# Kernel optimization log

Hardware: AMD Instinct MI355X
Metric: run time of the kernel (lower is better)

Reference implementation:

```python
import jax, jax.numpy as jnp
import numpy as np

N, E, G = 8192, 65536, 16          # nodes, edges, graphs
EMBED, HID, L = 512, 1024, 3       # embed_dim, hidden_dim, hidden_layers
NG, RBF_R = 50, 12.0               # num_gaussians, rbf_radius
AVG_LEN = 60.0
IN_DIM = 3 * EMBED


def _mlp_params(key, in_dim, hid, out_dim, n_layers):
    ks = jax.random.split(key, 6)
    s_in = 1.0 / np.sqrt(in_dim)
    s_h = 1.0 / np.sqrt(hid)
    return dict(
        in_w=jax.random.normal(ks[0], (in_dim, hid), jnp.float32) * s_in,
        in_b=jnp.zeros((hid,), jnp.float32),
        hid_w=jax.random.normal(ks[1], (n_layers, hid, hid), jnp.float32) * s_h,
        hid_b=jnp.zeros((n_layers, hid), jnp.float32),
        out_w=jax.random.normal(ks[2], (hid, out_dim), jnp.float32) * s_h,
        out_b=jnp.zeros((out_dim,), jnp.float32),
    )


def setup_inputs() -> dict:
    key = jax.random.key(0)
    k = jax.random.split(key, 8)
    x = jax.random.normal(k[0], (N, EMBED), jnp.float32)
    edge_index = jax.random.randint(k[1], (2, E), 0, N, dtype=jnp.int32)
    batch = jnp.sort(jax.random.randint(k[2], (N,), 0, G, dtype=jnp.int32))
    dist = jax.random.uniform(k[3], (E,), jnp.float32) * RBF_R
    v = jax.random.normal(k[4], (E, 3), jnp.float32)
    vec_hat = v / jnp.linalg.norm(v, axis=-1, keepdims=True)
    rbf_w = jax.random.normal(k[5], (NG, EMBED), jnp.float32) * (1.0 / np.sqrt(NG))
    rbf_b = jnp.zeros((EMBED,), jnp.float32)
    e = _mlp_params(k[6], IN_DIM, HID, 1, L)
    f = _mlp_params(k[7], IN_DIM, HID, 1, L)
    return dict(
        x=x, edge_index=edge_index, batch=batch, dist=dist, vec_hat=vec_hat,
        rbf_w=rbf_w, rbf_b=rbf_b,
        e_in_w=e['in_w'], e_in_b=e['in_b'], e_hid_w=e['hid_w'], e_hid_b=e['hid_b'], e_out_w=e['out_w'], e_out_b=e['out_b'],
        f_in_w=f['in_w'], f_in_b=f['in_b'], f_hid_w=f['hid_w'], f_hid_b=f['hid_b'], f_out_w=f['out_w'], f_out_b=f['out_b'],
    )


def _res_mlp(h_in, in_w, in_b, hid_w, hid_b, out_w, out_b):
    h = jax.nn.silu(h_in @ in_w + in_b)           # [E, HID]
    for i in range(L):                             # residual hidden blocks
        h = h + jax.nn.silu(h @ hid_w[i] + hid_b[i])
    return h @ out_w + out_b                       # [E, 1]


def _rbf(dist, rbf_w, rbf_b):
    offsets = jnp.linspace(0.0, RBF_R, NG)
    coeff = -0.5 / (offsets[1] - offsets[0]) ** 2
    g = jnp.exp(coeff * (dist[:, None] - offsets) ** 2)  # [E, NG]
    return g @ rbf_w + rbf_b                              # [E, EMBED]


def reference(x, edge_index, batch, dist, vec_hat,
              rbf_w, rbf_b,
              e_in_w, e_in_b, e_hid_w, e_hid_b, e_out_w, e_out_b,
              f_in_w, f_in_b, f_hid_w, f_hid_b, f_out_w, f_out_b):
    src, dst = edge_index[0], edge_index[1]
    rbf = _rbf(dist, rbf_w, rbf_b)                                 # [E, EMBED]
    inputs = jnp.concatenate([x[src], x[dst], rbf], axis=-1)       # [E, 3*EMBED]
    energy_pairs = _res_mlp(inputs, e_in_w, e_in_b, e_hid_w, e_hid_b, e_out_w, e_out_b)  # [E,1]
    force_pairs = _res_mlp(inputs, f_in_w, f_in_b, f_hid_w, f_hid_b, f_out_w, f_out_b) * vec_hat  # [E,3]
    energy = jax.ops.segment_sum(energy_pairs, batch[src], num_segments=G) / (AVG_LEN ** 2)  # [G,1]
    forces = jax.ops.segment_sum(force_pairs, src, num_segments=N) / AVG_LEN                 # [N,3]
    return energy, forces
```

## Files before the change

### kernel.cpp

```cpp
#include <hip/hip_runtime.h>
#include <math.h>

#define NUM_E 65536
#define NUM_N 8192
#define NUM_G 16
#define RBFR 12.0f

typedef unsigned short u16;
typedef _Float16 f16x8 __attribute__((ext_vector_type(8)));
typedef _Float16 f16x4 __attribute__((ext_vector_type(4)));
typedef float f32x4 __attribute__((ext_vector_type(4)));

#define TILE_F16 8192
#define L1SZ   1114112
#define HSZ    1048576
#define MSTRIDE 4259840

#define FU1  139264
#define FUHL 131072
#define FUPM (FU1 + 3 * FUHL)

#define GLD16(gp, lp) __builtin_amdgcn_global_load_lds( \
    (const __attribute__((address_space(1))) void*)(gp), \
    (__attribute__((address_space(3))) void*)(lp), 16, 0, 0)

#define VMW12() asm volatile("s_waitcnt vmcnt(12)" ::: "memory")
#define VMW10() asm volatile("s_waitcnt vmcnt(10)" ::: "memory")
#define VMW8()  asm volatile("s_waitcnt vmcnt(8)" ::: "memory")
#define VMW0()  asm volatile("s_waitcnt vmcnt(0)" ::: "memory")
#define BARX()  __builtin_amdgcn_s_barrier()

__global__ void wrbf_kernel(const float* __restrict__ rbf_w, const float* __restrict__ rbf_b,
                            const float* __restrict__ e_in_w, const float* __restrict__ e_in_b,
                            const float* __restrict__ f_in_w, const float* __restrict__ f_in_b,
                            float* __restrict__ wrbf_e, float* __restrict__ b1_e,
                            float* __restrict__ wrbf_f, float* __restrict__ b1_f) {
  int blk = blockIdx.x;
  int mlp = blk / 51;
  int row = blk % 51;
  const float* in_w = mlp ? f_in_w : e_in_w;
  const float* in_b = mlp ? f_in_b : e_in_b;
  float* wrbf = mlp ? wrbf_f : wrbf_e;
  float* b1   = mlp ? b1_f : b1_e;
  __shared__ float vec[512];
  for (int i = threadIdx.x; i < 512; i += 256)
    vec[i] = (row < 50) ? rbf_w[row * 512 + i] : rbf_b[i];
  __syncthreads();
  int n0 = threadIdx.x * 4;
  float a0 = 0.f, a1 = 0.f, a2 = 0.f, a3 = 0.f;
  for (int c = 0; c < 512; ++c) {
    const float4 wv = *(const float4*)&in_w[(size_t)(1024 + c) * 1024 + n0];
    float g = vec[c];
    a0 += g * wv.x; a1 += g * wv.y; a2 += g * wv.z; a3 += g * wv.w;
  }
  if (row < 50) {
    float4 o = {a0, a1, a2, a3};
    *(float4*)&wrbf[row * 1024 + n0] = o;
  } else {
    float4 o = {a0 + in_b[n0], a1 + in_b[n0 + 1], a2 + in_b[n0 + 2], a3 + in_b[n0 + 3]};
    *(float4*)&b1[n0] = o;
  }
}

__global__ void xh_kernel(const float* __restrict__ x, u16* __restrict__ xh) {
  int i = blockIdx.x * 256 + threadIdx.x;
  float4 v = ((const float4*)x)[i];
  f16x4 h = {(_Float16)v.x, (_Float16)v.y, (_Float16)v.z, (_Float16)v.w};
  *(f16x4*)(xh + (size_t)i * 4) = h;
}

__global__ void grbf_kernel(const float* __restrict__ dist, u16* __restrict__ grbf) {
  int u = blockIdx.x * 256 + threadIdx.x;
  int e = u >> 3, q = u & 7;
  const float delta = RBFR / 49.f;
  const float coeff = -0.5f / (delta * delta);
  float d = dist[e];
  f16x8 h;
#pragma unroll
  for (int j = 0; j < 8; ++j) {
    int gi = q * 8 + j;
    float dd = d - (float)gi * delta;
    float gg = (gi < 50) ? __expf(coeff * dd * dd) : 0.f;
    h[j] = (_Float16)gg;
  }
  *(f16x8*)(grbf + (size_t)u * 8) = h;
}

__global__ void pack_gemm(const float* __restrict__ e_in_w, const float* __restrict__ e_hid_w,
                          const float* __restrict__ f_in_w, const float* __restrict__ f_hid_w,
                          const float* __restrict__ wrbf_e, const float* __restrict__ wrbf_f,
                          u16* __restrict__ wp) {
  int u = blockIdx.x * 256 + threadIdx.x;
  if (u >= 2 * (MSTRIDE / 8)) return;
  int mlpi = (u >= MSTRIDE / 8) ? 1 : 0;
  int v = u - mlpi * (MSTRIDE / 8);
  const float* in_w  = mlpi ? f_in_w : e_in_w;
  const float* hid_w = mlpi ? f_hid_w : e_hid_w;
  const float* wrbf  = mlpi ? wrbf_f : wrbf_e;
  int t = v >> 10;
  int unit = v & 1023;
  int n_loc = unit >> 3;
  int sp = unit & 7;
  int ks = sp ^ (n_loc & 7);
  f16x8 vals;
  if (t < 136) {
    int grp = t / 17;
    int kt = t % 17;
    int bnp = grp >> 1, nhp = grp & 1;
    int n = bnp * 256 + ((n_loc >> 5) << 6) + nhp * 32 + (n_loc & 31);
    int k0 = kt * 64 + ks * 8;
#pragma unroll
    for (int j = 0; j < 8; ++j) {
      int k = k0 + j;
      float f = (k < 1024) ? in_w[(size_t)k * 1024 + n]
              : ((k < 1074) ? wrbf[(k - 1024) * 1024 + n] : 0.f);
      vals[j] = (_Float16)f;
    }
  } else {
    int th = t - 136;
    int lay = th >> 7;
    int t2 = th & 127;
    int bnp = t2 >> 5;
    int nhp = (t2 >> 4) & 1;
    int kt = t2 & 15;
    int n = bnp * 256 + ((n_loc >> 5) << 6) + nhp * 32 + (n_loc & 31);
    int k0 = kt * 64 + ks * 8;
#pragma unroll
    for (int j = 0; j < 8; ++j)
      vals[j] = (_Float16)hid_w[(size_t)((lay << 10) + k0 + j) * 1024 + n];
  }
  *(f16x8*)(wp + (size_t)mlpi * MSTRIDE + (size_t)t * TILE_F16 + unit * 8) = vals;
}


#define STA(b, ah, kt) do { \
  _Pragma("unroll") for (int _j = 0; _j < 2; ++_j) { \
    int _ck = wv * 2 + _j; \
    int _loc = _ck * 8 + (lane >> 3); \
    int _row = ((_loc >> 6) << 7) + (ah) * 64 + (_loc & 63); \
    int _sw = ((lane & 7) ^ (_loc & 7)) << 3; \
    const u16* _gp; \
    if (ISL1) { \
      if ((kt) < 16) { \
        int _nd = ((kt) < 8) ? s_src[_row] : s_dst[_row]; \
        _gp = hin + ((size_t)_nd * 512 + ((kt) & 7) * 64 + _sw); \
      } else { \
        _gp = grbf + ((size_t)(eg0 + _row) * 64 + _sw); \
      } \
    } else { \
      _gp = hin + ((size_t)(rowb + _row) * 1024 + (kt) * 64 + _sw); \
    } \
    GLD16(_gp, (char*)&sm[b][ah][0] + _ck * 1024); \
  } \
} while (0)

#define STB(b, bh, kt) do { \
  const u16* _wt = wl + ((size_t)((bn * 2 + (bh)) * NKT + (kt))) * TILE_F16; \
  _Pragma("unroll") for (int _j = 0; _j < 2; ++_j) { \
    int _ck = wv * 2 + _j; \
    GLD16(_wt + _ck * 512 + lane * 8, (char*)&sm[b][2 + (bh)][0] + _ck * 1024); \
  } \
} while (0)

#define RDA(b, mh) do { \
  _Pragma("unroll") for (int _ks = 0; _ks < 2; ++_ks) { \
    int _kk = _ks * 4 + (lane >> 4); \
    _Pragma("unroll") for (int _m = 0; _m < 4; ++_m) { \
      int _r = wm * 64 + _m * 16 + (lane & 15); \
      af[_m][_ks] = *(const f16x8*)&sm[b][mh][_r * 64 + ((_kk ^ (_r & 7)) << 3)]; \
    } \
  } \
} while (0)

#define RDB(b, nh) do { \
  _Pragma("unroll") for (int _ks = 0; _ks < 2; ++_ks) { \
    int _kk = _ks * 4 + (lane >> 4); \
    _Pragma("unroll") for (int _n = 0; _n < 2; ++_n) { \
      int _c = wn * 32 + _n * 16 + (lane & 15); \
      bf[nh][_n][_ks] = *(const f16x8*)&sm[b][2 + (nh)][_c * 64 + ((_kk ^ (_c & 7)) << 3)]; \
    } \
  } \
} while (0)

#define PHM(mh, nh) do { \
  __builtin_amdgcn_s_setprio(1); \
  _Pragma("unroll") for (int _ks = 0; _ks < 2; ++_ks) \
    _Pragma("unroll") for (int _m = 0; _m < 4; ++_m) \
      _Pragma("unroll") for (int _n = 0; _n < 2; ++_n) \
        acc[(mh) * 4 + _m][(nh) * 2 + _n] = __builtin_amdgcn_mfma_f32_16x16x32_f16( \
            bf[nh][_n][_ks], af[_m][_ks], acc[(mh) * 4 + _m][(nh) * 2 + _n], 0, 0, 0); \
  __builtin_amdgcn_s_setprio(0); \
} while (0)

template<int NKT, int ISL1>
__global__ __launch_bounds__(512, 2) void gemm8k(
    const u16* __restrict__ hin,
    const u16* __restrict__ grbf,
    const int* __restrict__ eidx,
    const u16* __restrict__ wl, const float* __restrict__ bias,
    u16* __restrict__ hout, int mstart) {
  __shared__ __align__(16) u16 sm[2][4][8192];
  __shared__ int s_src[256];
  __shared__ int s_dst[256];
  const int tid = threadIdx.x;
  const int lane = tid & 63;
  const int wv = tid >> 6;
  const int wm = wv >> 2, wn = wv & 3;
  const int g = (blockIdx.x & 7) * (gridDim.x >> 3) + (blockIdx.x >> 3);
  const int mt = g >> 2, bn = g & 3;
  const int rowb = mt * 256;
  const int n0 = bn * 256;
  const int eg0 = mstart + rowb;

  if (ISL1) {
    if (tid < 256) s_src[tid] = eidx[eg0 + tid];
    else s_dst[tid - 256] = eidx[NUM_E + eg0 + tid - 256];
    __syncthreads();
  }

  f32x4 acc[8][4];
#pragma unroll
  for (int m = 0; m < 8; ++m)
#pragma unroll
    for (int n = 0; n < 4; ++n)
#pragma unroll
      for (int i = 0; i < 4; ++i) acc[m][n][i] = 0.f;

  f16x8 af[4][2], bf[2][2][2];

  STA(0, 0, 0); STB(0, 0, 0); STB(0, 1, 0); STA(0, 1, 0);

  for (int t = 0; t < NKT - 1; ++t) {
    const int b = t & 1, nb = b ^ 1;
    STA(nb, 0, t + 1); STB(nb, 0, t + 1); STB(nb, 1, t + 1); STA(nb, 1, t + 1);
    VMW12(); BARX();
    RDA(b, 0); RDB(b, 0);
    PHM(0, 0); BARX();
    VMW10(); BARX();
    RDB(b, 1);
    PHM(0, 1); BARX();
    VMW8(); BARX();
    RDA(b, 1);
    PHM(1, 0); BARX();
    PHM(1, 1); BARX();
  }
  {
    const int tb = (NKT - 1) & 1;
    VMW0(); BARX();
    RDA(tb, 0); RDB(tb, 0); PHM(0, 0);
    RDB(tb, 1); PHM(0, 1);
    RDA(tb, 1); PHM(1, 0); PHM(1, 1);
  }

#pragma unroll
  for (int mi = 0; mi < 8; ++mi) {
#pragma unroll
    for (int ni = 0; ni < 4; ++ni) {
      int grow = rowb + wm * 128 + mi * 16 + (lane & 15);
      int gn = n0 + wn * 64 + ni * 16 + ((lane >> 4) << 2);
      float4 bi = *(const float4*)&bias[gn];
      f16x4 o;
      if (ISL1) {
#pragma unroll
        for (int i = 0; i < 4; ++i) {
          float pre = acc[mi][ni][i] + ((const float*)&bi)[i];
          o[i] = (_Float16)(pre / (1.f + __expf(-pre)));
        }
      } else {
        f16x4 hp = *(const f16x4*)&hin[(size_t)grow * 1024 + gn];
#pragma unroll
        for (int i = 0; i < 4; ++i) {
          float pre = acc[mi][ni][i] + ((const float*)&bi)[i];
          o[i] = (_Float16)(pre / (1.f + __expf(-pre)) + (float)hp[i]);
        }
      }
      *(f16x4*)&hout[(size_t)grow * 1024 + gn] = o;
    }
  }
}

__global__ void out_kernel(const u16* __restrict__ hfin, const int* __restrict__ eidx,
                           const int* __restrict__ batch, const float* __restrict__ vhat,
                           const float* __restrict__ ow, const float* __restrict__ ob,
                           float* __restrict__ out, int mstart, int isforce) {
  __shared__ float sow[1024];
  __shared__ float sbins[16];
  const int tid = threadIdx.x;
  if (tid < 16) sbins[tid] = 0.f;
  for (int i = tid; i < 1024; i += 512) sow[i] = ow[i];
  __syncthreads();
  int eloc = blockIdx.x * 64 + (tid >> 3);
  int part = tid & 7;
  float s = 0.f;
#pragma unroll
  for (int cc = 0; cc < 16; ++cc) {
    int col = part * 128 + cc * 8;
    f16x8 hv = *(const f16x8*)&hfin[(size_t)eloc * 1024 + col];
#pragma unroll
    for (int q = 0; q < 8; ++q) s += (float)hv[q] * sow[col + q];
  }
  s += __shfl_down(s, 4, 8);
  s += __shfl_down(s, 2, 8);
  s += __shfl_down(s, 1, 8);
  if (part == 0) {
    int eg = mstart + eloc;
    int si = eidx[eg];
    if (!isforce) {
      atomicAdd(&sbins[batch[si]], s + ob[0]);
    } else {
      float p = (s + ob[0]) * (1.f / 60.f);
      atomicAdd(&out[16 + si * 3 + 0], p * vhat[(size_t)eg * 3 + 0]);
      atomicAdd(&out[16 + si * 3 + 1], p * vhat[(size_t)eg * 3 + 1]);
      atomicAdd(&out[16 + si * 3 + 2], p * vhat[(size_t)eg * 3 + 2]);
    }
  }
  __syncthreads();
  if (!isforce && tid < 16) atomicAdd(&out[tid], sbins[tid] * (1.f / 3600.f));
}

#define FSWZ(row, col) ((((row) * 1088) + (col)) ^ (((row) & 7) << 3))

__global__ void packF_kernel(const float* __restrict__ e_in_w, const float* __restrict__ e_hid_w,
                             const float* __restrict__ f_in_w, const float* __restrict__ f_hid_w,
                             const float* __restrict__ wrbf_e, const float* __restrict__ wrbf_f,
                             u16* __restrict__ wp) {
  int u = blockIdx.x * 256 + threadIdx.x;
  if (u >= 2 * FUPM) return;
  int m = (u >= FUPM) ? 1 : 0;
  int v = u - m * FUPM;
  const float* in_w  = m ? f_in_w : e_in_w;
  const float* hid_w = m ? f_hid_w : e_hid_w;
  const float* wrbf  = m ? wrbf_f : wrbf_e;
  int l = v & 63;
  int kb = (l >> 4) << 3;
  f16x8 vals;
  if (v < FU1) {
    int kt = v >> 12;
    int ntg = (v >> 6) & 63;
    int n = ntg * 16 + (l & 15);
    int k0 = kt * 32 + kb;
#pragma unroll
    for (int jj = 0; jj < 8; ++jj) {
      int k = k0 + jj;
      float f = (k < 1024) ? in_w[(size_t)k * 1024 + n]
              : ((k < 1074) ? wrbf[(k - 1024) * 1024 + n] : 0.f);
      vals[jj] = (_Float16)f;
    }
  } else {
    int vh = v - FU1;
    int lay = vh >> 17;
    int kt = (vh >> 12) & 31;
    int ntg = (vh >> 6) & 63;
    int n = ntg * 16 + (l & 15);
    int k0 = kt * 32 + kb;
#pragma unroll
    for (int jj = 0; jj < 8; ++jj)
      vals[jj] = (_Float16)hid_w[(size_t)((lay << 10) + k0 + jj) * 1024 + n];
  }
  *(f16x8*)(wp + (size_t)u * 8) = vals;
}

#define F_LOADB(buf, kt) do { \
  const u16* _wr = wl + ((size_t)((kt) * 64 + wave * 8) * 64 + lane) * 8; \
  _Pragma("unroll") \
  for (int _nt = 0; _nt < 8; ++_nt) buf[_nt] = *(const f16x8*)(_wr + (size_t)_nt * 512); \
} while (0)
#define F_LOADA(buf, kt) do { \
  const int _kb = (kt) * 32 + ((lane >> 4) << 3); \
  _Pragma("unroll") \
  for (int _r = 0; _r < 4; ++_r) buf[_r] = *(const f16x8*)&Alds[FSWZ(_r * 16 + (lane & 15), _kb)]; \
} while (0)
#define F_MFMAS(abuf, bbuf) do { \
  _Pragma("unroll") \
  for (int _nt = 0; _nt < 8; ++_nt) \
    _Pragma("unroll") \
    for (int _r = 0; _r < 4; ++_r) \
      acc[_r][_nt] = __builtin_amdgcn_mfma_f32_16x16x32_f16(abuf[_r], bbuf[_nt], acc[_r][_nt], 0, 0, 0); \
} while (0)

__global__ __launch_bounds__(512, 2) void fusedF_kernel(
    const float* __restrict__ x, const int* __restrict__ eidx,
    const int* __restrict__ batch, const float* __restrict__ dist,
    const float* __restrict__ vhat,
    const u16* __restrict__ wp,
    const float* __restrict__ b1_e, const float* __restrict__ b1_f,
    const float* __restrict__ e_hid_b, const float* __restrict__ f_hid_b,
    const float* __restrict__ e_out_w, const float* __restrict__ e_out_b,
    const float* __restrict__ f_out_w, const float* __restrict__ f_out_b,
    float* __restrict__ out) {
  __shared__ __align__(16) u16 Alds[64 * 1088];
  __shared__ float sow[1024];
  __shared__ float sbins[16];
  __shared__ int s_src[64];
  __shared__ int s_dst[64];
  __shared__ float s_dist[64];
  const int tid = threadIdx.x;
  const int lane = tid & 63;
  const int wave = tid >> 6;
  const int e0 = blockIdx.x * 64;
  if (tid < 16) sbins[tid] = 0.f;
  if (tid < 64) s_src[tid] = eidx[e0 + tid];
  if (tid >= 64 && tid < 128) s_dst[tid - 64] = eidx[NUM_E + e0 + tid - 64];
  if (tid >= 128 && tid < 192) s_dist[tid - 128] = dist[e0 + tid - 128];
  __syncthreads();
  const float delta = RBFR / 49.f;
  const float coeff = -0.5f / (delta * delta);
  for (int mlp = 0; mlp < 2; ++mlp) {
    for (int i = tid; i < 16384; i += 512) {
      int e = i >> 8;
      int part = (i >> 7) & 1;
      int q = i & 127;
      int nrow = part ? s_dst[e] : s_src[e];
      float4 v = ((const float4*)x)[(size_t)nrow * 128 + q];
      int col = part * 512 + q * 4;
      f16x4 hv = {(_Float16)v.x, (_Float16)v.y, (_Float16)v.z, (_Float16)v.w};
      *(f16x4*)&Alds[FSWZ(e, col)] = hv;
    }
    for (int i = tid; i < 4096; i += 512) {
      int e = i >> 6;
      int gi = i & 63;
      float d = s_dist[e] - (float)gi * delta;
      float g2 = (gi < 50) ? __expf(coeff * d * d) : 0.f;
      _Float16 hg = (_Float16)g2;
      Alds[FSWZ(e, 1024 + gi)] = __builtin_bit_cast(u16, hg);
    }
    __syncthreads();
    const u16* wp1 = wp + (size_t)mlp * FUPM * 8;
    const u16* wph = wp1 + (size_t)FU1 * 8;
    const float* b1 = mlp ? b1_f : b1_e;
    const float* hb = mlp ? f_hid_b : e_hid_b;
    for (int layer = 0; layer < 4; ++layer) {
      const int nkt = (layer == 0) ? 34 : 32;
      const u16* wl = (layer == 0) ? wp1 : (wph + (size_t)(layer - 1) * FUHL * 8);
      const float* bias = (layer == 0) ? b1 : (hb + (layer - 1) * 1024);
      f32x4 acc[4][8];
#pragma unroll
      for (int r = 0; r < 4; ++r)
#pragma unroll
        for (int nt = 0; nt < 8; ++nt)
#pragma unroll
          for (int i = 0; i < 4; ++i) acc[r][nt][i] = 0.f;
      f16x8 a0[4], a1[4], b0[8], b1r[8];
      F_LOADA(a0, 0); F_LOADB(b0, 0);
      F_LOADA(a1, 1); F_LOADB(b1r, 1);
      for (int kt = 0; kt < nkt; kt += 2) {
        F_MFMAS(a0, b0);
        if (kt + 2 < nkt) { F_LOADA(a0, kt + 2); F_LOADB(b0, kt + 2); }
        F_MFMAS(a1, b1r);
        if (kt + 3 < nkt) { F_LOADA(a1, kt + 3); F_LOADB(b1r, kt + 3); }
      }
      __syncthreads();
      float bia[8];
#pragma unroll
      for (int nt = 0; nt < 8; ++nt) bia[nt] = bias[wave * 128 + nt * 16 + (lane & 15)];
#pragma unroll
      for (int r = 0; r < 4; ++r) {
#pragma unroll
        for (int nt = 0; nt < 8; ++nt) {
#pragma unroll
          for (int i = 0; i < 4; ++i) {
            int row = r * 16 + ((lane >> 4) << 2) + i;
            int col = wave * 128 + nt * 16 + (lane & 15);
            float pre = acc[r][nt][i] + bia[nt];
            float val = pre / (1.f + __expf(-pre));
            int idx = FSWZ(row, col);
            if (layer > 0) {
              _Float16 oldh = __builtin_bit_cast(_Float16, Alds[idx]);
              val += (float)oldh;
            }
            _Float16 nh = (_Float16)val;
            Alds[idx] = __builtin_bit_cast(u16, nh);
          }
        }
      }
      __syncthreads();
    }
    const float* ow = mlp ? f_out_w : e_out_w;
    for (int i = tid; i < 1024; i += 512) sow[i] = ow[i];
    __syncthreads();
    {
      int e = tid >> 3;
      int part = tid & 7;
      float s = 0.f;
#pragma unroll
      for (int cc = 0; cc < 16; ++cc) {
        int col = part * 128 + cc * 8;
        f16x8 hv = *(const f16x8*)&Alds[FSWZ(e, col)];
#pragma unroll
        for (int q = 0; q < 8; ++q) s += (float)hv[q] * sow[col + q];
      }
      s += __shfl_down(s, 4, 8);
      s += __shfl_down(s, 2, 8);
      s += __shfl_down(s, 1, 8);
      if (part == 0) {
        if (mlp == 0) {
          float p = s + e_out_b[0];
          int gg = batch[s_src[e]];
          atomicAdd(&sbins[gg], p);
        } else {
          float p = (s + f_out_b[0]) * (1.f / 60.f);
          int si = s_src[e];
          atomicAdd(&out[16 + si * 3 + 0], p * vhat[(size_t)(e0 + e) * 3 + 0]);
          atomicAdd(&out[16 + si * 3 + 1], p * vhat[(size_t)(e0 + e) * 3 + 1]);
          atomicAdd(&out[16 + si * 3 + 2], p * vhat[(size_t)(e0 + e) * 3 + 2]);
        }
      }
    }
    __syncthreads();
  }
  if (tid < 16) atomicAdd(&out[tid], sbins[tid] * (1.f / 3600.f));
}

extern "C" void kernel_launch(void* const* d_in, const int* in_sizes, int n_in,
                              void* d_out, int out_size, void* d_ws, size_t ws_size,
                              hipStream_t stream) {
  (void)in_sizes; (void)n_in;
  const float* x      = (const float*)d_in[0];
  const int*   eidx   = (const int*)d_in[1];
  const int*   batch  = (const int*)d_in[2];
  const float* dist   = (const float*)d_in[3];
  const float* vhat   = (const float*)d_in[4];
  const float* rbf_w  = (const float*)d_in[5];
  const float* rbf_b  = (const float*)d_in[6];
  const float* e_in_w = (const float*)d_in[7];
  const float* e_in_b = (const float*)d_in[8];
  const float* e_hid_w = (const float*)d_in[9];
  const float* e_hid_b = (const float*)d_in[10];
  const float* e_out_w = (const float*)d_in[11];
  const float* e_out_b = (const float*)d_in[12];
  const float* f_in_w = (const float*)d_in[13];
  const float* f_in_b = (const float*)d_in[14];
  const float* f_hid_w = (const float*)d_in[15];
  const float* f_hid_b = (const float*)d_in[16];
  const float* f_out_w = (const float*)d_in[17];
  const float* f_out_b = (const float*)d_in[18];

  const size_t WP_BYTES = 17039360;
  u16* wp       = (u16*)d_ws;
  float* wrbf_e = (float*)((char*)d_ws + WP_BYTES);
  float* wrbf_f = wrbf_e + 50 * 1024;
  float* b1_e   = wrbf_f + 50 * 1024;
  float* b1_f   = b1_e + 1024;
  const size_t BASE = WP_BYTES + 409600 + 8192;
  u16* xh   = (u16*)((char*)d_ws + BASE);
  u16* grbf = (u16*)((char*)d_ws + BASE + 8388608);
  const size_t FIXED = BASE + 16777216;

  int nch = 0;
  for (int c = 1; c <= 8; c <<= 1) {
    size_t need = FIXED + 2 * (size_t)(NUM_E / c) * 1024 * sizeof(u16);
    if (need <= ws_size) { nch = c; break; }
  }

  hipMemsetAsync(d_out, 0, (size_t)out_size * sizeof(float), stream);
  wrbf_kernel<<<102, 256, 0, stream>>>(rbf_w, rbf_b, e_in_w, e_in_b, f_in_w, f_in_b,
                                       wrbf_e, b1_e, wrbf_f, b1_f);

  if (nch == 0) {
    packF_kernel<<<(2 * FUPM + 255) / 256, 256, 0, stream>>>(
        e_in_w, e_hid_w, f_in_w, f_hid_w, wrbf_e, wrbf_f, wp);
    fusedF_kernel<<<NUM_E / 64, 512, 0, stream>>>(x, eidx, batch, dist, vhat, wp,
                                                  b1_e, b1_f, e_hid_b, f_hid_b,
                                                  e_out_w, e_out_b, f_out_w, f_out_b,
                                                  (float*)d_out);
    return;
  }

  pack_gemm<<<(2 * (MSTRIDE / 8) + 255) / 256, 256, 0, stream>>>(
      e_in_w, e_hid_w, f_in_w, f_hid_w, wrbf_e, wrbf_f, wp);
  xh_kernel<<<(NUM_N * 512 / 4) / 256, 256, 0, stream>>>(x, xh);
  grbf_kernel<<<(NUM_E * 8) / 256, 256, 0, stream>>>(dist, grbf);

  const int Mchunk = NUM_E / nch;
  const int nb256 = Mchunk / 256;
  u16* hA = (u16*)((char*)d_ws + FIXED);
  u16* hB = hA + (size_t)Mchunk * 1024;

  for (int c = 0; c < nch; ++c) {
    int mstart = c * Mchunk;
    for (int mlp = 0; mlp < 2; ++mlp) {
      const u16* wbase = wp + (size_t)mlp * MSTRIDE;
      const float* b1 = mlp ? b1_f : b1_e;
      const float* hb = mlp ? f_hid_b : e_hid_b;
      const float* ow = mlp ? f_out_w : e_out_w;
      const float* ob = mlp ? f_out_b : e_out_b;
      gemm8k<17, 1><<<nb256 * 4, 512, 0, stream>>>(xh, grbf, eidx, wbase, b1, hA, mstart);
      gemm8k<16, 0><<<nb256 * 4, 512, 0, stream>>>(hA, grbf, eidx, wbase + L1SZ, hb, hB, 0);
      gemm8k<16, 0><<<nb256 * 4, 512, 0, stream>>>(hB, grbf, eidx, wbase + L1SZ + HSZ, hb + 1024, hA, 0);
      gemm8k<16, 0><<<nb256 * 4, 512, 0, stream>>>(hA, grbf, eidx, wbase + L1SZ + 2 * HSZ, hb + 2048, hB, 0);
      out_kernel<<<Mchunk / 64, 512, 0, stream>>>(hB, eidx, batch, vhat, ow, ob,
                                                  (float*)d_out, mstart, mlp);
    }
  }
}
```

Before: 1.589 ms.

## Batch energy and force MLPs per GEMM launch and fuse output projection

```diff
diff --git a/kernel.cpp b/kernel.cpp
--- a/kernel.cpp
+++ b/kernel.cpp
@@ -36,29 +36,40 @@
                             float* __restrict__ wrbf_e, float* __restrict__ b1_e,
                             float* __restrict__ wrbf_f, float* __restrict__ b1_f) {
   int blk = blockIdx.x;
-  int mlp = blk / 51;
-  int row = blk % 51;
+  int mlp = blk / 204;
+  int rr = blk % 204;
+  int row = rr >> 2;
+  int ns = rr & 3;
   const float* in_w = mlp ? f_in_w : e_in_w;
   const float* in_b = mlp ? f_in_b : e_in_b;
   float* wrbf = mlp ? wrbf_f : wrbf_e;
   float* b1   = mlp ? b1_f : b1_e;
   __shared__ float vec[512];
-  for (int i = threadIdx.x; i < 512; i += 256)
-    vec[i] = (row < 50) ? rbf_w[row * 512 + i] : rbf_b[i];
+  __shared__ float4 red[256];
+  int tid = threadIdx.x;
+  vec[tid]       = (row < 50) ? rbf_w[row * 512 + tid]       : rbf_b[tid];
+  vec[tid + 256] = (row < 50) ? rbf_w[row * 512 + tid + 256] : rbf_b[tid + 256];
   __syncthreads();
-  int n0 = threadIdx.x * 4;
+  int q = tid >> 6, l = tid & 63;
+  int n0 = ns * 256 + l * 4;
   float a0 = 0.f, a1 = 0.f, a2 = 0.f, a3 = 0.f;
-  for (int c = 0; c < 512; ++c) {
-    const float4 wv = *(const float4*)&in_w[(size_t)(1024 + c) * 1024 + n0];
-    float g = vec[c];
-    a0 += g * wv.x; a1 += g * wv.y; a2 += g * wv.z; a3 += g * wv.w;
-  }
-  if (row < 50) {
-    float4 o = {a0, a1, a2, a3};
-    *(float4*)&wrbf[row * 1024 + n0] = o;
-  } else {
-    float4 o = {a0 + in_b[n0], a1 + in_b[n0 + 1], a2 + in_b[n0 + 2], a3 + in_b[n0 + 3]};
-    *(float4*)&b1[n0] = o;
+  for (int c = q * 128; c < q * 128 + 128; ++c) {
+    float4 wv = *(const float4*)&in_w[(size_t)(1024 + c) * 1024 + n0];
+    float gv = vec[c];
+    a0 += gv * wv.x; a1 += gv * wv.y; a2 += gv * wv.z; a3 += gv * wv.w;
+  }
+  red[tid] = float4{a0, a1, a2, a3};
+  __syncthreads();
+  if (q == 0) {
+    float4 s0 = red[l], s1 = red[l + 64], s2 = red[l + 128], s3 = red[l + 192];
+    float4 o = {s0.x + s1.x + s2.x + s3.x, s0.y + s1.y + s2.y + s3.y,
+                s0.z + s1.z + s2.z + s3.z, s0.w + s1.w + s2.w + s3.w};
+    if (row < 50) {
+      *(float4*)&wrbf[row * 1024 + n0] = o;
+    } else {
+      o.x += in_b[n0]; o.y += in_b[n0 + 1]; o.z += in_b[n0 + 2]; o.w += in_b[n0 + 3];
+      *(float4*)&b1[n0] = o;
+    }
   }
 }
 
@@ -140,7 +151,7 @@
     int _row = ((_loc >> 6) << 7) + (ah) * 64 + (_loc & 63); \
     int _sw = ((lane & 7) ^ (_loc & 7)) << 3; \
     const u16* _gp; \
-    if (ISL1) { \
+    if (MODE == 1) { \
       if ((kt) < 16) { \
         int _nd = ((kt) < 8) ? s_src[_row] : s_dst[_row]; \
         _gp = hin + ((size_t)_nd * 512 + ((kt) & 7) * 64 + _sw); \
@@ -192,27 +203,50 @@
   __builtin_amdgcn_s_setprio(0); \
 } while (0)
 
-template<int NKT, int ISL1>
+template<int NKT, int MODE>
 __global__ __launch_bounds__(512, 2) void gemm8k(
-    const u16* __restrict__ hin,
-    const u16* __restrict__ grbf,
-    const int* __restrict__ eidx,
-    const u16* __restrict__ wl, const float* __restrict__ bias,
-    u16* __restrict__ hout, int mstart) {
+    const u16* __restrict__ hinE, const u16* __restrict__ hinF,
+    const u16* __restrict__ grbf, const int* __restrict__ eidx,
+    const int* __restrict__ batch, const float* __restrict__ vhat,
+    const u16* __restrict__ wp, size_t woff,
+    const float* __restrict__ biasE, const float* __restrict__ biasF,
+    u16* __restrict__ houtE, u16* __restrict__ houtF,
+    const float* __restrict__ owE, const float* __restrict__ owF,
+    const float* __restrict__ obE, const float* __restrict__ obF,
+    float* __restrict__ out, int mstart) {
   __shared__ __align__(16) u16 sm[2][4][8192];
   __shared__ int s_src[256];
   __shared__ int s_dst[256];
+  __shared__ float sred[256];
+  __shared__ float sbins[16];
   const int tid = threadIdx.x;
   const int lane = tid & 63;
   const int wv = tid >> 6;
   const int wm = wv >> 2, wn = wv & 3;
-  const int g = (blockIdx.x & 7) * (gridDim.x >> 3) + (blockIdx.x >> 3);
-  const int mt = g >> 2, bn = g & 3;
+
+  int mlp, mt, bn;
+  if (MODE == 1) {
+    int g = (blockIdx.x & 7) * (gridDim.x >> 3) + (blockIdx.x >> 3);
+    mt = g >> 3;
+    int bnq = g & 7;
+    mlp = bnq >> 2;
+    bn = bnq & 3;
+  } else {
+    mlp = blockIdx.x & 1;
+    int b2 = blockIdx.x >> 1;
+    int g = (b2 & 7) * ((gridDim.x >> 1) >> 3) + (b2 >> 3);
+    mt = g >> 2;
+    bn = g & 3;
+  }
+  const u16* hin = (MODE == 1) ? hinE : (mlp ? hinF : hinE);
+  const u16* wl = wp + (size_t)mlp * MSTRIDE + woff;
+  const float* bias = mlp ? biasF : biasE;
+  u16* hout = mlp ? houtF : houtE;
   const int rowb = mt * 256;
   const int n0 = bn * 256;
   const int eg0 = mstart + rowb;
 
-  if (ISL1) {
+  if (MODE == 1) {
     if (tid < 256) s_src[tid] = eidx[eg0 + tid];
     else s_dst[tid - 256] = eidx[NUM_E + eg0 + tid - 256];
     __syncthreads();
@@ -252,70 +286,85 @@
     RDA(tb, 1); PHM(1, 0); PHM(1, 1);
   }
 
-#pragma unroll
-  for (int mi = 0; mi < 8; ++mi) {
-#pragma unroll
-    for (int ni = 0; ni < 4; ++ni) {
-      int grow = rowb + wm * 128 + mi * 16 + (lane & 15);
-      int gn = n0 + wn * 64 + ni * 16 + ((lane >> 4) << 2);
-      float4 bi = *(const float4*)&bias[gn];
-      f16x4 o;
-      if (ISL1) {
+  if (MODE != 2) {
+#pragma unroll
+    for (int mi = 0; mi < 8; ++mi) {
+#pragma unroll
+      for (int ni = 0; ni < 4; ++ni) {
+        int grow = rowb + wm * 128 + mi * 16 + (lane & 15);
+        int gn = n0 + wn * 64 + ni * 16 + ((lane >> 4) << 2);
+        float4 bi = *(const float4*)&bias[gn];
+        f16x4 o;
+        if (MODE == 1) {
+#pragma unroll
+          for (int i = 0; i < 4; ++i) {
+            float pre = acc[mi][ni][i] + ((const float*)&bi)[i];
+            o[i] = (_Float16)(pre / (1.f + __expf(-pre)));
+          }
+        } else {
+          f16x4 hp = *(const f16x4*)&hin[(size_t)grow * 1024 + gn];
+#pragma unroll
+          for (int i = 0; i < 4; ++i) {
+            float pre = acc[mi][ni][i] + ((const float*)&bi)[i];
+            o[i] = (_Float16)(pre / (1.f + __expf(-pre)) + (float)hp[i]);
+          }
+        }
+        *(f16x4*)&hout[(size_t)grow * 1024 + gn] = o;
+      }
+    }
+  } else {
+    if (tid < 256) sred[tid] = 0.f;
+    if (tid < 16) sbins[tid] = 0.f;
+    __syncthreads();
+    const float* ow = mlp ? owF : owE;
+    float p[8];
+#pragma unroll
+    for (int mi = 0; mi < 8; ++mi) p[mi] = 0.f;
+#pragma unroll
+    for (int mi = 0; mi < 8; ++mi) {
+#pragma unroll
+      for (int ni = 0; ni < 4; ++ni) {
+        int grow = rowb + wm * 128 + mi * 16 + (lane & 15);
+        int gn = n0 + wn * 64 + ni * 16 + ((lane >> 4) << 2);
+        float4 bi = *(const float4*)&bias[gn];
+        float4 wv4 = *(const float4*)&ow[gn];
+        f16x4 hp = *(const f16x4*)&hin[(size_t)grow * 1024 + gn];
 #pragma unroll
         for (int i = 0; i < 4; ++i) {
           float pre = acc[mi][ni][i] + ((const float*)&bi)[i];
-          o[i] = (_Float16)(pre / (1.f + __expf(-pre)));
-        }
-      } else {
-        f16x4 hp = *(const f16x4*)&hin[(size_t)grow * 1024 + gn];
-#pragma unroll
-        for (int i = 0; i < 4; ++i) {
-          float pre = acc[mi][ni][i] + ((const float*)&bi)[i];
-          o[i] = (_Float16)(pre / (1.f + __expf(-pre)) + (float)hp[i]);
+          float val = pre / (1.f + __expf(-pre)) + (float)hp[i];
+          p[mi] += val * ((const float*)&wv4)[i];
         }
       }
-      *(f16x4*)&hout[(size_t)grow * 1024 + gn] = o;
-    }
-  }
-}
-
-__global__ void out_kernel(const u16* __restrict__ hfin, const int* __restrict__ eidx,
-                           const int* __restrict__ batch, const float* __restrict__ vhat,
-                           const float* __restrict__ ow, const float* __restrict__ ob,
-                           float* __restrict__ out, int mstart, int isforce) {
-  __shared__ float sow[1024];
-  __shared__ float sbins[16];
-  const int tid = threadIdx.x;
-  if (tid < 16) sbins[tid] = 0.f;
-  for (int i = tid; i < 1024; i += 512) sow[i] = ow[i];
-  __syncthreads();
-  int eloc = blockIdx.x * 64 + (tid >> 3);
-  int part = tid & 7;
-  float s = 0.f;
-#pragma unroll
-  for (int cc = 0; cc < 16; ++cc) {
-    int col = part * 128 + cc * 8;
-    f16x8 hv = *(const f16x8*)&hfin[(size_t)eloc * 1024 + col];
-#pragma unroll
-    for (int q = 0; q < 8; ++q) s += (float)hv[q] * sow[col + q];
-  }
-  s += __shfl_down(s, 4, 8);
-  s += __shfl_down(s, 2, 8);
-  s += __shfl_down(s, 1, 8);
-  if (part == 0) {
-    int eg = mstart + eloc;
-    int si = eidx[eg];
-    if (!isforce) {
-      atomicAdd(&sbins[batch[si]], s + ob[0]);
-    } else {
-      float p = (s + ob[0]) * (1.f / 60.f);
-      atomicAdd(&out[16 + si * 3 + 0], p * vhat[(size_t)eg * 3 + 0]);
-      atomicAdd(&out[16 + si * 3 + 1], p * vhat[(size_t)eg * 3 + 1]);
-      atomicAdd(&out[16 + si * 3 + 2], p * vhat[(size_t)eg * 3 + 2]);
-    }
-  }
-  __syncthreads();
-  if (!isforce && tid < 16) atomicAdd(&out[tid], sbins[tid] * (1.f / 3600.f));
+    }
+#pragma unroll
+    for (int mi = 0; mi < 8; ++mi) {
+      p[mi] += __shfl_down(p[mi], 32, 64);
+      p[mi] += __shfl_down(p[mi], 16, 64);
+    }
+    if ((lane >> 4) == 0) {
+#pragma unroll
+      for (int mi = 0; mi < 8; ++mi)
+        atomicAdd(&sred[wm * 128 + mi * 16 + (lane & 15)], p[mi]);
+    }
+    __syncthreads();
+    if (tid < 256) {
+      float s = sred[tid];
+      int eg = eg0 + tid;
+      int si = eidx[eg];
+      if (mlp == 0) {
+        float pv = s + ((bn == 0) ? obE[0] : 0.f);
+        atomicAdd(&sbins[batch[si]], pv);
+      } else {
+        float pv = (s + ((bn == 0) ? obF[0] : 0.f)) * (1.f / 60.f);
+        atomicAdd(&out[16 + si * 3 + 0], pv * vhat[(size_t)eg * 3 + 0]);
+        atomicAdd(&out[16 + si * 3 + 1], pv * vhat[(size_t)eg * 3 + 1]);
+        atomicAdd(&out[16 + si * 3 + 2], pv * vhat[(size_t)eg * 3 + 2]);
+      }
+    }
+    __syncthreads();
+    if (mlp == 0 && tid < 16) atomicAdd(&out[tid], sbins[tid] * (1.f / 3600.f));
+  }
 }
 
 #define FSWZ(row, col) ((((row) * 1088) + (col)) ^ (((row) & 7) << 3))
@@ -494,15 +543,15 @@
       s += __shfl_down(s, 1, 8);
       if (part == 0) {
         if (mlp == 0) {
-          float p = s + e_out_b[0];
+          float pp = s + e_out_b[0];
           int gg = batch[s_src[e]];
-          atomicAdd(&sbins[gg], p);
+          atomicAdd(&sbins[gg], pp);
         } else {
-          float p = (s + f_out_b[0]) * (1.f / 60.f);
+          float pp = (s + f_out_b[0]) * (1.f / 60.f);
           int si = s_src[e];
-          atomicAdd(&out[16 + si * 3 + 0], p * vhat[(size_t)(e0 + e) * 3 + 0]);
-          atomicAdd(&out[16 + si * 3 + 1], p * vhat[(size_t)(e0 + e) * 3 + 1]);
-          atomicAdd(&out[16 + si * 3 + 2], p * vhat[(size_t)(e0 + e) * 3 + 2]);
+          atomicAdd(&out[16 + si * 3 + 0], pp * vhat[(size_t)(e0 + e) * 3 + 0]);
+          atomicAdd(&out[16 + si * 3 + 1], pp * vhat[(size_t)(e0 + e) * 3 + 1]);
+          atomicAdd(&out[16 + si * 3 + 2], pp * vhat[(size_t)(e0 + e) * 3 + 2]);
         }
       }
     }
@@ -548,12 +597,12 @@
 
   int nch = 0;
   for (int c = 1; c <= 8; c <<= 1) {
-    size_t need = FIXED + 2 * (size_t)(NUM_E / c) * 1024 * sizeof(u16);
+    size_t need = FIXED + 4 * (size_t)(NUM_E / c) * 1024 * sizeof(u16);
     if (need <= ws_size) { nch = c; break; }
   }
 
   hipMemsetAsync(d_out, 0, (size_t)out_size * sizeof(float), stream);
-  wrbf_kernel<<<102, 256, 0, stream>>>(rbf_w, rbf_b, e_in_w, e_in_b, f_in_w, f_in_b,
+  wrbf_kernel<<<408, 256, 0, stream>>>(rbf_w, rbf_b, e_in_w, e_in_b, f_in_w, f_in_b,
                                        wrbf_e, b1_e, wrbf_f, b1_f);
 
   if (nch == 0) {
@@ -572,24 +621,26 @@
   grbf_kernel<<<(NUM_E * 8) / 256, 256, 0, stream>>>(dist, grbf);
 
   const int Mchunk = NUM_E / nch;
-  const int nb256 = Mchunk / 256;
-  u16* hA = (u16*)((char*)d_ws + FIXED);
-  u16* hB = hA + (size_t)Mchunk * 1024;
+  u16* hE0 = (u16*)((char*)d_ws + FIXED);
+  u16* hE1 = hE0 + (size_t)Mchunk * 1024;
+  u16* hF0 = hE1 + (size_t)Mchunk * 1024;
+  u16* hF1 = hF0 + (size_t)Mchunk * 1024;
+  float* out = (float*)d_out;
 
   for (int c = 0; c < nch; ++c) {
     int mstart = c * Mchunk;
-    for (int mlp = 0; mlp < 2; ++mlp) {
-      const u16* wbase = wp + (size_t)mlp * MSTRIDE;
-      const float* b1 = mlp ? b1_f : b1_e;
-      const float* hb = mlp ? f_hid_b : e_hid_b;
-      const float* ow = mlp ? f_out_w : e_out_w;
-      const float* ob = mlp ? f_out_b : e_out_b;
-      gemm8k<17, 1><<<nb256 * 4, 512, 0, stream>>>(xh, grbf, eidx, wbase, b1, hA, mstart);
-      gemm8k<16, 0><<<nb256 * 4, 512, 0, stream>>>(hA, grbf, eidx, wbase + L1SZ, hb, hB, 0);
-      gemm8k<16, 0><<<nb256 * 4, 512, 0, stream>>>(hB, grbf, eidx, wbase + L1SZ + HSZ, hb + 1024, hA, 0);
-      gemm8k<16, 0><<<nb256 * 4, 512, 0, stream>>>(hA, grbf, eidx, wbase + L1SZ + 2 * HSZ, hb + 2048, hB, 0);
-      out_kernel<<<Mchunk / 64, 512, 0, stream>>>(hB, eidx, batch, vhat, ow, ob,
-                                                  (float*)d_out, mstart, mlp);
-    }
-  }
-}
+    int grid = Mchunk / 32;
+    gemm8k<17, 1><<<grid, 512, 0, stream>>>(
+        xh, xh, grbf, eidx, batch, vhat, wp, 0,
+        b1_e, b1_f, hE0, hF0, e_out_w, f_out_w, e_out_b, f_out_b, out, mstart);
+    gemm8k<16, 0><<<grid, 512, 0, stream>>>(
+        hE0, hF0, grbf, eidx, batch, vhat, wp, L1SZ,
+        e_hid_b, f_hid_b, hE1, hF1, e_out_w, f_out_w, e_out_b, f_out_b, out, mstart);
+    gemm8k<16, 0><<<grid, 512, 0, stream>>>(
+        hE1, hF1, grbf, eidx, batch, vhat, wp, L1SZ + HSZ,
+        e_hid_b + 1024, f_hid_b + 1024, hE0, hF0, e_out_w, f_out_w, e_out_b, f_out_b, out, mstart);
+    gemm8k<16, 2><<<grid, 512, 0, stream>>>(
+        hE0, hF0, grbf, eidx, batch, vhat, wp, L1SZ + 2 * HSZ,
+        e_hid_b + 2048, f_hid_b + 2048, hE1, hF1, e_out_w, f_out_w, e_out_b, f_out_b, out, mstart);
+  }
+}
```

Result: faster. 1.555 ms (-2.2%).
